# Performance work log

Hardware: AMD Instinct MI355X
Metric: run time of the kernel (lower is better)

The kernel has to match this reference:

```python
import jax, jax.numpy as jnp
import numpy as np

H = 2048      # hidden_size
I = 8192      # dense intermediate_size
MI = 1024     # moe_intermediate_size
E = 8         # num_local_experts
K = 2         # num_experts_per_tok
B, S = 2, 1024
EPS = 1e-6
ROOT = H ** (-0.5)


def _rms(x, w=None, eps=EPS):
    # fp32 RMSNorm matching _Gemma4CPURMSNorm; w=None -> no-scale variant
    ms = jnp.mean(x * x, axis=-1, keepdims=True) + eps
    y = x * jax.lax.rsqrt(ms)
    return y * w if w is not None else y


def _gelu_tanh(x):
    # gelu_pytorch_tanh == tanh-approximate gelu
    return jax.nn.gelu(x, approximate=True)


def setup_inputs() -> dict:
    key = jax.random.key(0)
    ks = jax.random.split(key, 10)
    s = 0.02
    return {
        "hidden_states": jax.random.normal(ks[0], (B, S, H), jnp.float32),
        # RMSNorm scales (init ones, as in nn.Parameter(torch.ones(dim)))
        "rn_pre1": jnp.ones((H,), jnp.float32),
        "rn_pre2": jnp.ones((H,), jnp.float32),
        "rn_post1": jnp.ones((H,), jnp.float32),
        "rn_post2": jnp.ones((H,), jnp.float32),
        "rn_post": jnp.ones((H,), jnp.float32),
        # dense GLU MLP weights, stored (in, out)
        "w_gate": jax.random.normal(ks[1], (H, I), jnp.float32) * s,
        "w_up":   jax.random.normal(ks[2], (H, I), jnp.float32) * s,
        "w_down": jax.random.normal(ks[3], (I, H), jnp.float32) * s,
        # router
        "router_w": jax.random.normal(ks[4], (H, E), jnp.float32) * s,
        "router_scale": jnp.ones((H,), jnp.float32),
        "per_expert_scale": jnp.ones((E,), jnp.float32),
        # per-expert GLU weights, stacked over experts
        "we_gate": jax.random.normal(ks[5], (E, H, MI), jnp.float32) * s,
        "we_up":   jax.random.normal(ks[6], (E, H, MI), jnp.float32) * s,
        "we_down": jax.random.normal(ks[7], (E, MI, H), jnp.float32) * s,
    }


def reference(hidden_states, rn_pre1, rn_pre2, rn_post1, rn_post2, rn_post,
              w_gate, w_up, w_down, router_w, router_scale, per_expert_scale,
              we_gate, we_up, we_down):
    b, s, h = hidden_states.shape
    T = b * s

    # --- dense branch ---
    dense_in = _rms(hidden_states, rn_pre1)                      # (B,S,H)
    dense_out = (_gelu_tanh(dense_in @ w_gate) * (dense_in @ w_up)) @ w_down
    dense_out = _rms(dense_out, rn_post1)                        # (B,S,H)

    # --- router (takes the raw residual, applies its own no-scale RMSNorm) ---
    x = hidden_states.reshape(T, h)
    xr = _rms(x) * router_scale * ROOT                           # (T,H)
    router_logits = xr @ router_w                                # (T,E)
    probs = jax.nn.softmax(router_logits, axis=-1)
    top_w, top_i = jax.lax.top_k(probs, K)                       # (T,K)
    top_w = top_w / jnp.sum(top_w, axis=-1, keepdims=True)
    top_w = top_w * per_expert_scale[top_i]
    aff = jnp.zeros((T, E), x.dtype).at[jnp.arange(T)[:, None], top_i].set(top_w)

    # --- MoE experts (compute all experts, combine with sparse affinities) ---
    moe_in = _rms(hidden_states, rn_pre2).reshape(T, h)          # (T,H)
    g = jnp.einsum('th,ehm->tem', moe_in, we_gate)               # (T,E,MI)
    u = jnp.einsum('th,ehm->tem', moe_in, we_up)
    eo = jnp.einsum('tem,emh->teh', _gelu_tanh(g) * u, we_down)  # (T,E,H)
    moe_out = jnp.einsum('te,teh->th', aff, eo).reshape(b, s, h)
    moe_out = _rms(moe_out, rn_post2)

    return _rms(dense_out + moe_out, rn_post)
```

## Files before the change

kernel.cpp:

```cpp
#include <hip/hip_runtime.h>
#include <stdint.h>

#define TOK 2048
#define HD  2048
#define ID  8192
#define ID2 16384
#define MID 1024
#define NE  8
#define KSPLIT 4

typedef __attribute__((ext_vector_type(8))) short s16x8;
typedef __attribute__((ext_vector_type(4))) short s16x4;
typedef __attribute__((ext_vector_type(4))) float f32x4;

constexpr float EPSF  = 1e-6f;
constexpr float ROOTF = 0.02209708691207961f;

#define MFMA(a, b, c) __builtin_amdgcn_mfma_f32_16x16x32_bf16(a, b, c, 0, 0, 0)
#define BAR() __builtin_amdgcn_s_barrier()
#define SCHED0() __builtin_amdgcn_sched_barrier(0)
#define VMCNT(n) asm volatile("s_waitcnt vmcnt(" #n ")" ::: "memory")

__device__ __forceinline__ void gload16(const void* g, void* l) {
  __builtin_amdgcn_global_load_lds(
      (const __attribute__((address_space(1))) void*)g,
      (__attribute__((address_space(3))) void*)l, 16, 0, 0);
}

__device__ __forceinline__ short f2bf(float f) {
  union { float f; uint32_t u; } v; v.f = f;
  uint32_t r = v.u + 0x7fffu + ((v.u >> 16) & 1u);
  return (short)(r >> 16);
}

__device__ __forceinline__ float bf2f(short s) {
  union { uint32_t u; float f; } v; v.u = ((uint32_t)(uint16_t)s) << 16;
  return v.f;
}

__device__ __forceinline__ float gelu_tanh(float x) {
  float x3 = x * x * x;
  float u = 0.7978845608028654f * (x + 0.044715f * x3);
  return 0.5f * x * (1.0f + tanhf(u));
}

__global__ __launch_bounds__(256) void k_rms_router(
    const float* __restrict__ x, const float* __restrict__ rnp1,
    const float* __restrict__ rnp2, const float* __restrict__ rsc,
    const float* __restrict__ rw, const float* __restrict__ pes,
    short* __restrict__ rms1, short* __restrict__ rms2,
    int* __restrict__ cnt, int* __restrict__ tokl,
    float* __restrict__ wgtl, int* __restrict__ slotl) {
  const int t = blockIdx.x, tid = threadIdx.x;
  const size_t base = (size_t)t * HD;
  f32x4 v[2];
  float ss = 0.f;
#pragma unroll
  for (int i = 0; i < 2; ++i) {
    v[i] = *(const f32x4*)(x + base + tid * 4 + i * 1024);
#pragma unroll
    for (int j = 0; j < 4; ++j) ss += v[i][j] * v[i][j];
  }
  __shared__ float sr[4];
  __shared__ float sl[32];
#pragma unroll
  for (int off = 32; off; off >>= 1) ss += __shfl_down(ss, off, 64);
  if ((tid & 63) == 0) sr[tid >> 6] = ss;
  __syncthreads();
  const float inv = rsqrtf((sr[0] + sr[1] + sr[2] + sr[3]) * (1.0f / HD) + EPSF);
  float p[8] = {0, 0, 0, 0, 0, 0, 0, 0};
#pragma unroll
  for (int i = 0; i < 2; ++i) {
    const int h = tid * 4 + i * 1024;
    f32x4 w1 = *(const f32x4*)(rnp1 + h);
    f32x4 w2 = *(const f32x4*)(rnp2 + h);
    f32x4 sc = *(const f32x4*)(rsc + h);
    s16x4 o1, o2;
#pragma unroll
    for (int j = 0; j < 4; ++j) {
      float xn = v[i][j] * inv;
      o1[j] = f2bf(xn * w1[j]);
      o2[j] = f2bf(xn * w2[j]);
      float xq = xn * sc[j] * ROOTF;
      const float* rr = rw + (size_t)(h + j) * NE;
      f32x4 ra = *(const f32x4*)rr;
      f32x4 rb = *(const f32x4*)(rr + 4);
      p[0] += xq * ra[0]; p[1] += xq * ra[1]; p[2] += xq * ra[2]; p[3] += xq * ra[3];
      p[4] += xq * rb[0]; p[5] += xq * rb[1]; p[6] += xq * rb[2]; p[7] += xq * rb[3];
    }
    *(s16x4*)(rms1 + base + h) = o1;
    *(s16x4*)(rms2 + base + h) = o2;
  }
#pragma unroll
  for (int e = 0; e < 8; ++e)
#pragma unroll
    for (int off = 32; off; off >>= 1) p[e] += __shfl_down(p[e], off, 64);
  if ((tid & 63) == 0) {
#pragma unroll
    for (int e = 0; e < 8; ++e) sl[(tid >> 6) * 8 + e] = p[e];
  }
  __syncthreads();
  if (tid == 0) {
    float l[8];
#pragma unroll
    for (int e = 0; e < 8; ++e) l[e] = sl[e] + sl[8 + e] + sl[16 + e] + sl[24 + e];
    int i1 = 0;
#pragma unroll
    for (int e = 1; e < 8; ++e) if (l[e] > l[i1]) i1 = e;
    int i2 = (i1 == 0) ? 1 : 0;
#pragma unroll
    for (int e = 0; e < 8; ++e) if (e != i1 && l[e] > l[i2]) i2 = e;
    float p2 = expf(l[i2] - l[i1]);
    float s = 1.0f + p2;
    float w1 = (1.0f / s) * pes[i1];
    float w2 = (p2 / s) * pes[i2];
    int q1 = atomicAdd(&cnt[i1], 1);
    tokl[i1 * TOK + q1] = t; wgtl[i1 * TOK + q1] = w1; slotl[i1 * TOK + q1] = 0;
    int q2 = atomicAdd(&cnt[i2], 1);
    tokl[i2 * TOK + q2] = t; wgtl[i2 * TOK + q2] = w2; slotl[i2 * TOK + q2] = 1;
  }
}

__global__ __launch_bounds__(256) void k_transpose(
    const float* __restrict__ in, short* __restrict__ out, int R, int C) {
  __shared__ float tile[64 * 65];
  const int tid = threadIdx.x;
  const int c0 = blockIdx.x * 64, r0 = blockIdx.y * 64;
  const size_t bo = (size_t)blockIdx.z * R * C;
#pragma unroll
  for (int i = 0; i < 4; ++i) {
    int idx = tid + 256 * i;
    int r = idx >> 4, c4 = idx & 15;
    f32x4 f = *(const f32x4*)(in + bo + (size_t)(r0 + r) * C + c0 + c4 * 4);
#pragma unroll
    for (int j = 0; j < 4; ++j) tile[(c4 * 4 + j) * 65 + r] = f[j];
  }
  __syncthreads();
#pragma unroll
  for (int i = 0; i < 2; ++i) {
    int ch = tid + 256 * i;
    int c = ch >> 3, rs = ch & 7;
    s16x8 o;
#pragma unroll
    for (int q = 0; q < 8; ++q) o[q] = f2bf(tile[c * 65 + rs * 8 + q]);
    *(s16x8*)(out + bo + (size_t)(c0 + c) * R + r0 + rs * 8) = o;
  }
}

__global__ __launch_bounds__(512, 2) void k_gemm256(
    const short* __restrict__ Wt,
    const short* __restrict__ X,
    short* __restrict__ C) {
  __shared__ char lds[2][65536];
  const int tid = threadIdx.x;
  const int lane = tid & 63, wave = tid >> 6;
  const int wr = wave >> 2, wc = wave & 3;
  const int ln15 = lane & 15, l16 = lane >> 4;
  const int m0 = blockIdx.x * 256, t0 = blockIdx.y * 256;
  const int swz = (ln15 & 7) << 4;
  const int srow = tid >> 3;
  const int sslot = ((tid & 7) ^ ((tid >> 3) & 7)) << 4;
  const char* Wb = (const char*)Wt;
  const char* Xb = (const char*)X;
  auto STAGE = [&](int kt, int s) {
#pragma unroll
    for (int c = 0; c < 4; ++c) {
      gload16(Wb + (size_t)(m0 + c * 64 + srow) * 4096 + kt * 128 + sslot,
              &lds[s][c * 8192] + wave * 1024);
      gload16(Xb + (size_t)(t0 + c * 64 + srow) * 4096 + kt * 128 + sslot,
              &lds[s][32768 + c * 8192] + wave * 1024);
    }
  };
  f32x4 acc[8][4];
#pragma unroll
  for (int m = 0; m < 8; ++m)
#pragma unroll
    for (int n = 0; n < 4; ++n) acc[m][n] = (f32x4)0.f;
  const int NT = HD / 64;
  STAGE(0, 0);
  STAGE(1, 1);
  VMCNT(8);
  SCHED0();
  BAR();
#pragma unroll 2
  for (int kt = 0; kt < NT; ++kt) {
    const int s = kt & 1;
    const char* sA = &lds[s][0];
    const char* sB = &lds[s][32768];
#pragma unroll
    for (int mh = 0; mh < 2; ++mh)
#pragma unroll
      for (int ks = 0; ks < 2; ++ks) {
        const int ka = (ks * 64 + l16 * 16) ^ swz;
        s16x8 a[4], b[4];
#pragma unroll
        for (int f = 0; f < 4; ++f)
          a[f] = *(const s16x8*)(sA + (wr * 128 + mh * 64 + f * 16 + ln15) * 128 + ka);
#pragma unroll
        for (int n = 0; n < 4; ++n)
          b[n] = *(const s16x8*)(sB + (wc * 64 + n * 16 + ln15) * 128 + ka);
        __builtin_amdgcn_s_setprio(1);
#pragma unroll
        for (int f = 0; f < 4; ++f)
#pragma unroll
          for (int n = 0; n < 4; ++n)
            acc[mh * 4 + f][n] = MFMA(a[f], b[n], acc[mh * 4 + f][n]);
        __builtin_amdgcn_s_setprio(0);
      }
    BAR();
    if (kt + 2 < NT) {
      STAGE(kt + 2, s);
      VMCNT(8);
    } else if (kt + 1 < NT) {
      VMCNT(0);
    }
    SCHED0();
    BAR();
  }
#pragma unroll
  for (int mi = 0; mi < 8; ++mi)
#pragma unroll
    for (int n = 0; n < 4; ++n) {
      const int t = t0 + wc * 64 + n * 16 + ln15;
      const int i = m0 + wr * 128 + mi * 16 + l16 * 4;
      s16x4 o;
#pragma unroll
      for (int r = 0; r < 4; ++r) o[r] = f2bf(acc[mi][n][r]);
      *(s16x4*)(C + (size_t)t * ID2 + i) = o;
    }
}

__global__ __launch_bounds__(512, 2) void k_dd256(
    const short* __restrict__ Wd,
    const short* __restrict__ X,
    float* __restrict__ dparts) {
  __shared__ char lds[2][65536];
  const int tid = threadIdx.x;
  const int lane = tid & 63, wave = tid >> 6;
  const int wr = wave >> 2, wc = wave & 3;
  const int ln15 = lane & 15, l16 = lane >> 4;
  const int m0 = blockIdx.x * 256, t0 = blockIdx.y * 256;
  const size_t kB = (size_t)blockIdx.z * 4096;
  const int swz = (ln15 & 7) << 4;
  const int srow = tid >> 3;
  const int sslot = ((tid & 7) ^ ((tid >> 3) & 7)) << 4;
  const char* Wb = (const char*)Wd;
  const char* Xb = (const char*)X;
  auto STAGE = [&](int kt, int s) {
#pragma unroll
    for (int c = 0; c < 4; ++c) {
      gload16(Wb + (size_t)(m0 + c * 64 + srow) * 16384 + kB + kt * 128 + sslot,
              &lds[s][c * 8192] + wave * 1024);
      gload16(Xb + (size_t)(t0 + c * 64 + srow) * 16384 + kB + kt * 128 + sslot,
              &lds[s][32768 + c * 8192] + wave * 1024);
    }
  };
  f32x4 acc[8][4];
#pragma unroll
  for (int m = 0; m < 8; ++m)
#pragma unroll
    for (int n = 0; n < 4; ++n) acc[m][n] = (f32x4)0.f;
  const int NT = (ID / KSPLIT) / 64;
  STAGE(0, 0);
  STAGE(1, 1);
  VMCNT(8);
  SCHED0();
  BAR();
#pragma unroll 2
  for (int kt = 0; kt < NT; ++kt) {
    const int s = kt & 1;
    const char* sA = &lds[s][0];
    const char* sB = &lds[s][32768];
#pragma unroll
    for (int mh = 0; mh < 2; ++mh)
#pragma unroll
      for (int ks = 0; ks < 2; ++ks) {
        const int ka = (ks * 64 + l16 * 16) ^ swz;
        s16x8 a[4], b[4];
#pragma unroll
        for (int f = 0; f < 4; ++f)
          a[f] = *(const s16x8*)(sA + (wr * 128 + mh * 64 + f * 16 + ln15) * 128 + ka);
#pragma unroll
        for (int n = 0; n < 4; ++n)
          b[n] = *(const s16x8*)(sB + (wc * 64 + n * 16 + ln15) * 128 + ka);
        __builtin_amdgcn_s_setprio(1);
#pragma unroll
        for (int f = 0; f < 4; ++f)
#pragma unroll
          for (int n = 0; n < 4; ++n)
            acc[mh * 4 + f][n] = MFMA(a[f], b[n], acc[mh * 4 + f][n]);
        __builtin_amdgcn_s_setprio(0);
      }
    BAR();
    if (kt + 2 < NT) {
      STAGE(kt + 2, s);
      VMCNT(8);
    } else if (kt + 1 < NT) {
      VMCNT(0);
    }
    SCHED0();
    BAR();
  }
  float* dst = dparts + (size_t)blockIdx.z * TOK * HD;
#pragma unroll
  for (int mi = 0; mi < 8; ++mi)
#pragma unroll
    for (int n = 0; n < 4; ++n) {
      const int t = t0 + wc * 64 + n * 16 + ln15;
      const int h = m0 + wr * 128 + mi * 16 + l16 * 4;
      *(f32x4*)(dst + (size_t)t * HD + h) = acc[mi][n];
    }
}

__global__ __launch_bounds__(256) void k_gelumul(
    const short* __restrict__ cbuf, short* __restrict__ o) {
  const int flat = blockIdx.x * 256 + threadIdx.x;
  const int t = flat >> 10;
  const int i8 = (flat & 1023) * 8;
  const short* g = cbuf + (size_t)t * ID2 + i8;
  s16x8 gv = *(const s16x8*)g;
  s16x8 uv = *(const s16x8*)(g + ID);
  s16x8 ov;
#pragma unroll
  for (int j = 0; j < 8; ++j)
    ov[j] = f2bf(gelu_tanh(bf2f(gv[j])) * bf2f(uv[j]));
  *(s16x8*)(o + (size_t)t * ID + i8) = ov;
}

__global__ __launch_bounds__(256) void k_exp_gateup(
    const short* __restrict__ wegT, const short* __restrict__ weuT,
    const short* __restrict__ rms2,
    const int* __restrict__ cnt, const int* __restrict__ tokl,
    short* __restrict__ acte) {
  const int e = blockIdx.z;
  const int cn = cnt[e];
  const int t0 = blockIdx.y * 128;
  if (t0 >= cn) return;
  const int n0 = blockIdx.x * 64;
  __shared__ short sW[128 * 32];
  __shared__ short sX[128 * 32];
  const int tid = threadIdx.x;
  const int lane = tid & 63, wave = tid >> 6;
  const int ln15 = lane & 15, k8 = (lane >> 4) * 8;
  const int nsub = (wave & 1) * 32, tsub = (wave >> 1) * 64;
  const int srow = tid >> 2, skc = (tid & 3) * 8;
  const int* tl = tokl + e * TOK;
  int r0 = t0 + srow, r1 = t0 + 64 + srow;
  int tk0 = tl[r0 < cn ? r0 : cn - 1];
  int tk1 = tl[r1 < cn ? r1 : cn - 1];
  const short* gW0 = wegT + (size_t)e * MID * HD + (size_t)(n0 + srow) * HD + skc;
  const short* gW1 = weuT + (size_t)e * MID * HD + (size_t)(n0 + srow) * HD + skc;
  const short* gX0 = rms2 + (size_t)tk0 * HD + skc;
  const short* gX1 = rms2 + (size_t)tk1 * HD + skc;
  char* lW = (char*)sW + wave * 1024;
  char* lX = (char*)sX + wave * 1024;
  f32x4 accg[2][4], accu[2][4];
#pragma unroll
  for (int m = 0; m < 2; ++m)
#pragma unroll
    for (int n = 0; n < 4; ++n) { accg[m][n] = (f32x4)0.f; accu[m][n] = (f32x4)0.f; }
  for (int kt = 0; kt < HD / 32; ++kt) {
    const int ko = kt * 32;
    __syncthreads();
    gload16(gW0 + ko, lW);
    gload16(gW1 + ko, lW + 4096);
    gload16(gX0 + ko, lX);
    gload16(gX1 + ko, lX + 4096);
    __syncthreads();
    s16x8 ag[2], au[2], bx[4];
#pragma unroll
    for (int m = 0; m < 2; ++m) {
      ag[m] = *(const s16x8*)(sW + (nsub + m * 16 + ln15) * 32 + k8);
      au[m] = *(const s16x8*)(sW + (64 + nsub + m * 16 + ln15) * 32 + k8);
    }
#pragma unroll
    for (int n = 0; n < 4; ++n)
      bx[n] = *(const s16x8*)(sX + (tsub + n * 16 + ln15) * 32 + k8);
#pragma unroll
    for (int m = 0; m < 2; ++m)
#pragma unroll
      for (int n = 0; n < 4; ++n) {
        accg[m][n] = MFMA(ag[m], bx[n], accg[m][n]);
        accu[m][n] = MFMA(au[m], bx[n], accu[m][n]);
      }
  }
#pragma unroll
  for (int m = 0; m < 2; ++m)
#pragma unroll
    for (int n = 0; n < 4; ++n) {
      const int r = t0 + tsub + n * 16 + ln15;
      if (r < cn) {
        const int ib = n0 + nsub + m * 16 + (lane >> 4) * 4;
        s16x4 o;
#pragma unroll
        for (int q = 0; q < 4; ++q)
          o[q] = f2bf(gelu_tanh(accg[m][n][q]) * accu[m][n][q]);
        *(s16x4*)(acte + (size_t)e * TOK * MID + (size_t)r * MID + ib) = o;
      }
    }
}

__global__ __launch_bounds__(256) void k_exp_down(
    const short* __restrict__ wedT,
    const short* __restrict__ acte,
    const int* __restrict__ cnt, const int* __restrict__ tokl,
    const float* __restrict__ wgtl, const int* __restrict__ slotl,
    float* __restrict__ moep) {
  const int e = blockIdx.z;
  const int cn = cnt[e];
  const int t0 = blockIdx.y * 128;
  if (t0 >= cn) return;
  const int n0 = blockIdx.x * 128;
  __shared__ short sW[128 * 32];
  __shared__ short sX[128 * 32];
  const int tid = threadIdx.x;
  const int lane = tid & 63, wave = tid >> 6;
  const int wr = wave >> 1, wc = wave & 1;
  const int ln15 = lane & 15, k8 = (lane >> 4) * 8;
  const int srow = tid >> 2, skc = (tid & 3) * 8;
  const short* wb = wedT + (size_t)e * HD * MID;
  const short* gW0 = wb + (size_t)(n0 + srow) * MID + skc;
  const short* gW1 = wb + (size_t)(n0 + 64 + srow) * MID + skc;
  const short* ab = acte + (size_t)e * TOK * MID;
  const short* gX0 = ab + (size_t)(t0 + srow) * MID + skc;
  const short* gX1 = ab + (size_t)(t0 + 64 + srow) * MID + skc;
  char* lW = (char*)sW + wave * 1024;
  char* lX = (char*)sX + wave * 1024;
  f32x4 acc[4][4];
#pragma unroll
  for (int m = 0; m < 4; ++m)
#pragma unroll
    for (int n = 0; n < 4; ++n) acc[m][n] = (f32x4)0.f;
  for (int kt = 0; kt < MID / 32; ++kt) {
    const int ko = kt * 32;
    __syncthreads();
    gload16(gW0 + ko, lW);
    gload16(gW1 + ko, lW + 4096);
    gload16(gX0 + ko, lX);
    gload16(gX1 + ko, lX + 4096);
    __syncthreads();
    s16x8 a[4], b[4];
#pragma unroll
    for (int m = 0; m < 4; ++m)
      a[m] = *(const s16x8*)(sW + (wr * 64 + m * 16 + ln15) * 32 + k8);
#pragma unroll
    for (int n = 0; n < 4; ++n)
      b[n] = *(const s16x8*)(sX + (wc * 64 + n * 16 + ln15) * 32 + k8);
#pragma unroll
    for (int m = 0; m < 4; ++m)
#pragma unroll
      for (int n = 0; n < 4; ++n) acc[m][n] = MFMA(a[m], b[n], acc[m][n]);
  }
#pragma unroll
  for (int n = 0; n < 4; ++n) {
    const int r = t0 + wc * 64 + n * 16 + ln15;
    if (r < cn) {
      const int tk = tokl[e * TOK + r];
      const float wf = wgtl[e * TOK + r];
      const int sl = slotl[e * TOK + r];
      float* dst = moep + (size_t)sl * TOK * HD + (size_t)tk * HD;
#pragma unroll
      for (int m = 0; m < 4; ++m) {
        const int h = n0 + wr * 64 + m * 16 + (lane >> 4) * 4;
        f32x4 v = acc[m][n] * wf;
        *(f32x4*)(dst + h) = v;
      }
    }
  }
}

__global__ __launch_bounds__(256) void k_final(
    const float* __restrict__ dparts, const float* __restrict__ moep,
    const float* __restrict__ rno1, const float* __restrict__ rno2,
    const float* __restrict__ rnof, float* __restrict__ out) {
  const int t = blockIdx.x, tid = threadIdx.x;
  const size_t base = (size_t)t * HD;
  f32x4 dv[2], mv[2];
  float ssd = 0.f, ssm = 0.f;
#pragma unroll
  for (int i = 0; i < 2; ++i) {
    const int h = tid * 4 + i * 1024;
    dv[i] = (f32x4)0.f;
#pragma unroll
    for (int z = 0; z < KSPLIT; ++z)
      dv[i] += *(const f32x4*)(dparts + (size_t)z * TOK * HD + base + h);
    f32x4 a = *(const f32x4*)(moep + base + h);
    f32x4 b = *(const f32x4*)(moep + (size_t)TOK * HD + base + h);
    mv[i] = a + b;
#pragma unroll
    for (int j = 0; j < 4; ++j) { ssd += dv[i][j] * dv[i][j]; ssm += mv[i][j] * mv[i][j]; }
  }
  __shared__ float sr[8];
#pragma unroll
  for (int off = 32; off; off >>= 1) {
    ssd += __shfl_down(ssd, off, 64);
    ssm += __shfl_down(ssm, off, 64);
  }
  if ((tid & 63) == 0) { sr[tid >> 6] = ssd; sr[4 + (tid >> 6)] = ssm; }
  __syncthreads();
  const float invd = rsqrtf((sr[0] + sr[1] + sr[2] + sr[3]) * (1.0f / HD) + EPSF);
  const float invm = rsqrtf((sr[4] + sr[5] + sr[6] + sr[7]) * (1.0f / HD) + EPSF);
  f32x4 y[2];
  float ssy = 0.f;
#pragma unroll
  for (int i = 0; i < 2; ++i) {
    const int h = tid * 4 + i * 1024;
    f32x4 w1 = *(const f32x4*)(rno1 + h);
    f32x4 w2 = *(const f32x4*)(rno2 + h);
#pragma unroll
    for (int j = 0; j < 4; ++j) {
      y[i][j] = dv[i][j] * invd * w1[j] + mv[i][j] * invm * w2[j];
      ssy += y[i][j] * y[i][j];
    }
  }
  __syncthreads();
#pragma unroll
  for (int off = 32; off; off >>= 1) ssy += __shfl_down(ssy, off, 64);
  if ((tid & 63) == 0) sr[tid >> 6] = ssy;
  __syncthreads();
  const float invy = rsqrtf((sr[0] + sr[1] + sr[2] + sr[3]) * (1.0f / HD) + EPSF);
#pragma unroll
  for (int i = 0; i < 2; ++i) {
    const int h = tid * 4 + i * 1024;
    f32x4 w = *(const f32x4*)(rnof + h);
    f32x4 o;
#pragma unroll
    for (int j = 0; j < 4; ++j) o[j] = y[i][j] * invy * w[j];
    *(f32x4*)(out + base + h) = o;
  }
}

extern "C" void kernel_launch(void* const* d_in, const int* in_sizes, int n_in,
                              void* d_out, int out_size, void* d_ws, size_t ws_size,
                              hipStream_t stream) {
  (void)in_sizes; (void)n_in; (void)out_size;
  const float* x    = (const float*)d_in[0];
  const float* rnp1 = (const float*)d_in[1];
  const float* rnp2 = (const float*)d_in[2];
  const float* rno1 = (const float*)d_in[3];
  const float* rno2 = (const float*)d_in[4];
  const float* rnof = (const float*)d_in[5];
  const float* wg   = (const float*)d_in[6];
  const float* wu   = (const float*)d_in[7];
  const float* wd   = (const float*)d_in[8];
  const float* rw   = (const float*)d_in[9];
  const float* rsc  = (const float*)d_in[10];
  const float* pes  = (const float*)d_in[11];
  const float* weg  = (const float*)d_in[12];
  const float* weu  = (const float*)d_in[13];
  const float* wed  = (const float*)d_in[14];
  float* out = (float*)d_out;

  char* ws = (char*)d_ws;
  size_t off = 0;
  auto alloc = [&](size_t bytes) -> void* {
    void* p = ws + off;
    off += (bytes + 255) & ~(size_t)255;
    return p;
  };
  const size_t IH  = (size_t)ID * HD;
  const size_t EMH = (size_t)NE * MID * HD;
  short* wgT   = (short*)alloc(IH * 2);
  short* wuT   = (short*)alloc(IH * 2);
  short* wdT   = (short*)alloc(IH * 2);
  short* wegT  = (short*)alloc(EMH * 2);
  short* weuT  = (short*)alloc(EMH * 2);
  short* wedT  = (short*)alloc(EMH * 2);
  short* rms1  = (short*)alloc((size_t)TOK * HD * 2);
  short* rms2  = (short*)alloc((size_t)TOK * HD * 2);
  short* actb  = (short*)alloc((size_t)TOK * ID * 2);
  short* acte  = (short*)alloc((size_t)NE * TOK * MID * 2);
  float* moep  = (float*)alloc((size_t)2 * TOK * HD * 4);
  int*   cnt   = (int*)alloc(NE * 4);
  int*   tokl  = (int*)alloc((size_t)NE * TOK * 4);
  float* wgtl  = (float*)alloc((size_t)NE * TOK * 4);
  int*   slotl = (int*)alloc((size_t)NE * TOK * 4);
  if (off > ws_size) return;
  float* dparts = (float*)wgT;
  short* cbuf = acte;

  hipMemsetAsync(cnt, 0, NE * 4, stream);
  k_rms_router<<<TOK, 256, 0, stream>>>(x, rnp1, rnp2, rsc, rw, pes,
                                        rms1, rms2, cnt, tokl, wgtl, slotl);
  k_transpose<<<dim3(ID / 64, HD / 64, 1), 256, 0, stream>>>(wg, wgT, HD, ID);
  k_transpose<<<dim3(ID / 64, HD / 64, 1), 256, 0, stream>>>(wu, wuT, HD, ID);
  k_transpose<<<dim3(HD / 64, ID / 64, 1), 256, 0, stream>>>(wd, wdT, ID, HD);
  k_transpose<<<dim3(MID / 64, HD / 64, NE), 256, 0, stream>>>(weg, wegT, HD, MID);
  k_transpose<<<dim3(MID / 64, HD / 64, NE), 256, 0, stream>>>(weu, weuT, HD, MID);
  k_transpose<<<dim3(HD / 64, MID / 64, NE), 256, 0, stream>>>(wed, wedT, MID, HD);
  k_gemm256<<<dim3(ID2 / 256, TOK / 256), 512, 0, stream>>>(wgT, rms1, cbuf);
  k_gelumul<<<(TOK * ID) / (256 * 8), 256, 0, stream>>>(cbuf, actb);
  k_dd256<<<dim3(HD / 256, TOK / 256, KSPLIT), 512, 0, stream>>>(wdT, actb, dparts);
  k_exp_gateup<<<dim3(MID / 64, TOK / 128, NE), 256, 0, stream>>>(wegT, weuT, rms2,
                                                                  cnt, tokl, acte);
  k_exp_down<<<dim3(HD / 128, TOK / 128, NE), 256, 0, stream>>>(wedT, acte, cnt, tokl,
                                                                wgtl, slotl, moep);
  k_final<<<TOK, 256, 0, stream>>>(dparts, moep, rno1, rno2, rnof, out);
}
```

Measured before the change: 551.5 us.

## Port expert GEMMs to 256x256 pipelined MFMA kernels and store dense split-K partials as bf16

Replaces the small 128-tile expert gate/up and down kernels with 256x256, 512-thread, double-buffered, swizzled-LDS GEMMs modeled on the dense path. Gate and up now run as two launches, with the second fusing gelu*up into its epilogue by reading back a bf16 gate buffer. The inner loop in all big GEMMs is reordered so B fragments load once per k-step, and the dense split-K partials are written in bf16 instead of fp32 to halve that traffic. The costs are bf16 rounding of partial sums, an extra gate-buffer round trip, and many idle 256-token tiles for experts with few tokens.

```diff
diff --git a/kernel.cpp b/kernel.cpp
--- a/kernel.cpp
+++ b/kernel.cpp
@@ -188,17 +188,18 @@
     const char* sA = &lds[s][0];
     const char* sB = &lds[s][32768];
 #pragma unroll
-    for (int mh = 0; mh < 2; ++mh)
-#pragma unroll
-      for (int ks = 0; ks < 2; ++ks) {
-        const int ka = (ks * 64 + l16 * 16) ^ swz;
-        s16x8 a[4], b[4];
+    for (int ks = 0; ks < 2; ++ks) {
+      const int ka = (ks * 64 + l16 * 16) ^ swz;
+      s16x8 b[4];
+#pragma unroll
+      for (int n = 0; n < 4; ++n)
+        b[n] = *(const s16x8*)(sB + (wc * 64 + n * 16 + ln15) * 128 + ka);
+#pragma unroll
+      for (int mh = 0; mh < 2; ++mh) {
+        s16x8 a[4];
 #pragma unroll
         for (int f = 0; f < 4; ++f)
           a[f] = *(const s16x8*)(sA + (wr * 128 + mh * 64 + f * 16 + ln15) * 128 + ka);
-#pragma unroll
-        for (int n = 0; n < 4; ++n)
-          b[n] = *(const s16x8*)(sB + (wc * 64 + n * 16 + ln15) * 128 + ka);
         __builtin_amdgcn_s_setprio(1);
 #pragma unroll
         for (int f = 0; f < 4; ++f)
@@ -207,6 +208,7 @@
             acc[mh * 4 + f][n] = MFMA(a[f], b[n], acc[mh * 4 + f][n]);
         __builtin_amdgcn_s_setprio(0);
       }
+    }
     BAR();
     if (kt + 2 < NT) {
       STAGE(kt + 2, s);
@@ -233,7 +235,7 @@
 __global__ __launch_bounds__(512, 2) void k_dd256(
     const short* __restrict__ Wd,
     const short* __restrict__ X,
-    float* __restrict__ dparts) {
+    short* __restrict__ dparts) {
   __shared__ char lds[2][65536];
   const int tid = threadIdx.x;
   const int lane = tid & 63, wave = tid >> 6;
@@ -272,17 +274,18 @@
     const char* sA = &lds[s][0];
     const char* sB = &lds[s][32768];
 #pragma unroll
-    for (int mh = 0; mh < 2; ++mh)
-#pragma unroll
-      for (int ks = 0; ks < 2; ++ks) {
-        const int ka = (ks * 64 + l16 * 16) ^ swz;
-        s16x8 a[4], b[4];
+    for (int ks = 0; ks < 2; ++ks) {
+      const int ka = (ks * 64 + l16 * 16) ^ swz;
+      s16x8 b[4];
+#pragma unroll
+      for (int n = 0; n < 4; ++n)
+        b[n] = *(const s16x8*)(sB + (wc * 64 + n * 16 + ln15) * 128 + ka);
+#pragma unroll
+      for (int mh = 0; mh < 2; ++mh) {
+        s16x8 a[4];
 #pragma unroll
         for (int f = 0; f < 4; ++f)
           a[f] = *(const s16x8*)(sA + (wr * 128 + mh * 64 + f * 16 + ln15) * 128 + ka);
-#pragma unroll
-        for (int n = 0; n < 4; ++n)
-          b[n] = *(const s16x8*)(sB + (wc * 64 + n * 16 + ln15) * 128 + ka);
         __builtin_amdgcn_s_setprio(1);
 #pragma unroll
         for (int f = 0; f < 4; ++f)
@@ -291,6 +294,7 @@
             acc[mh * 4 + f][n] = MFMA(a[f], b[n], acc[mh * 4 + f][n]);
         __builtin_amdgcn_s_setprio(0);
       }
+    }
     BAR();
     if (kt + 2 < NT) {
       STAGE(kt + 2, s);
@@ -301,14 +305,17 @@
     SCHED0();
     BAR();
   }
-  float* dst = dparts + (size_t)blockIdx.z * TOK * HD;
+  short* dst = dparts + (size_t)blockIdx.z * TOK * HD;
 #pragma unroll
   for (int mi = 0; mi < 8; ++mi)
 #pragma unroll
     for (int n = 0; n < 4; ++n) {
       const int t = t0 + wc * 64 + n * 16 + ln15;
       const int h = m0 + wr * 128 + mi * 16 + l16 * 4;
-      *(f32x4*)(dst + (size_t)t * HD + h) = acc[mi][n];
+      s16x4 o;
+#pragma unroll
+      for (int r = 0; r < 4; ++r) o[r] = f2bf(acc[mi][n][r]);
+      *(s16x4*)(dst + (size_t)t * HD + h) = o;
     }
 }
 
@@ -327,129 +334,193 @@
   *(s16x8*)(o + (size_t)t * ID + i8) = ov;
 }
 
-__global__ __launch_bounds__(256) void k_exp_gateup(
-    const short* __restrict__ wegT, const short* __restrict__ weuT,
-    const short* __restrict__ rms2,
+__global__ __launch_bounds__(512, 2) void k_eg256(
+    const short* __restrict__ W,
+    const short* __restrict__ X,
     const int* __restrict__ cnt, const int* __restrict__ tokl,
-    short* __restrict__ acte) {
+    short* __restrict__ gout,
+    short* __restrict__ aout,
+    int fuse) {
+  __shared__ char lds[2][65536];
   const int e = blockIdx.z;
   const int cn = cnt[e];
-  const int t0 = blockIdx.y * 128;
+  const int t0 = blockIdx.y * 256;
   if (t0 >= cn) return;
-  const int n0 = blockIdx.x * 64;
-  __shared__ short sW[128 * 32];
-  __shared__ short sX[128 * 32];
   const int tid = threadIdx.x;
   const int lane = tid & 63, wave = tid >> 6;
-  const int ln15 = lane & 15, k8 = (lane >> 4) * 8;
-  const int nsub = (wave & 1) * 32, tsub = (wave >> 1) * 64;
-  const int srow = tid >> 2, skc = (tid & 3) * 8;
+  const int wr = wave >> 2, wc = wave & 3;
+  const int ln15 = lane & 15, l16 = lane >> 4;
+  const int m0 = blockIdx.x * 256;
+  const int swz = (ln15 & 7) << 4;
+  const int srow = tid >> 3;
+  const int sslot = ((tid & 7) ^ ((tid >> 3) & 7)) << 4;
+  const char* Wb = (const char*)(W + (size_t)e * MID * HD + (size_t)m0 * HD);
+  const char* Xb = (const char*)X;
   const int* tl = tokl + e * TOK;
-  int r0 = t0 + srow, r1 = t0 + 64 + srow;
-  int tk0 = tl[r0 < cn ? r0 : cn - 1];
-  int tk1 = tl[r1 < cn ? r1 : cn - 1];
-  const short* gW0 = wegT + (size_t)e * MID * HD + (size_t)(n0 + srow) * HD + skc;
-  const short* gW1 = weuT + (size_t)e * MID * HD + (size_t)(n0 + srow) * HD + skc;
-  const short* gX0 = rms2 + (size_t)tk0 * HD + skc;
-  const short* gX1 = rms2 + (size_t)tk1 * HD + skc;
-  char* lW = (char*)sW + wave * 1024;
-  char* lX = (char*)sX + wave * 1024;
-  f32x4 accg[2][4], accu[2][4];
-#pragma unroll
-  for (int m = 0; m < 2; ++m)
-#pragma unroll
-    for (int n = 0; n < 4; ++n) { accg[m][n] = (f32x4)0.f; accu[m][n] = (f32x4)0.f; }
-  for (int kt = 0; kt < HD / 32; ++kt) {
-    const int ko = kt * 32;
-    __syncthreads();
-    gload16(gW0 + ko, lW);
-    gload16(gW1 + ko, lW + 4096);
-    gload16(gX0 + ko, lX);
-    gload16(gX1 + ko, lX + 4096);
-    __syncthreads();
-    s16x8 ag[2], au[2], bx[4];
-#pragma unroll
-    for (int m = 0; m < 2; ++m) {
-      ag[m] = *(const s16x8*)(sW + (nsub + m * 16 + ln15) * 32 + k8);
-      au[m] = *(const s16x8*)(sW + (64 + nsub + m * 16 + ln15) * 32 + k8);
-    }
-#pragma unroll
-    for (int n = 0; n < 4; ++n)
-      bx[n] = *(const s16x8*)(sX + (tsub + n * 16 + ln15) * 32 + k8);
-#pragma unroll
-    for (int m = 0; m < 2; ++m)
-#pragma unroll
-      for (int n = 0; n < 4; ++n) {
-        accg[m][n] = MFMA(ag[m], bx[n], accg[m][n]);
-        accu[m][n] = MFMA(au[m], bx[n], accu[m][n]);
+  int tk[4];
+#pragma unroll
+  for (int c = 0; c < 4; ++c) {
+    int r = t0 + c * 64 + srow;
+    tk[c] = tl[r < cn ? r : cn - 1];
+  }
+  auto STAGE = [&](int kt, int s) {
+#pragma unroll
+    for (int c = 0; c < 4; ++c) {
+      gload16(Wb + (size_t)(c * 64 + srow) * 4096 + kt * 128 + sslot,
+              &lds[s][c * 8192] + wave * 1024);
+      gload16(Xb + (size_t)tk[c] * 4096 + kt * 128 + sslot,
+              &lds[s][32768 + c * 8192] + wave * 1024);
+    }
+  };
+  f32x4 acc[8][4];
+#pragma unroll
+  for (int m = 0; m < 8; ++m)
+#pragma unroll
+    for (int n = 0; n < 4; ++n) acc[m][n] = (f32x4)0.f;
+  const int NT = HD / 64;
+  STAGE(0, 0);
+  STAGE(1, 1);
+  VMCNT(8);
+  SCHED0();
+  BAR();
+#pragma unroll 2
+  for (int kt = 0; kt < NT; ++kt) {
+    const int s = kt & 1;
+    const char* sA = &lds[s][0];
+    const char* sB = &lds[s][32768];
+#pragma unroll
+    for (int ks = 0; ks < 2; ++ks) {
+      const int ka = (ks * 64 + l16 * 16) ^ swz;
+      s16x8 b[4];
+#pragma unroll
+      for (int n = 0; n < 4; ++n)
+        b[n] = *(const s16x8*)(sB + (wc * 64 + n * 16 + ln15) * 128 + ka);
+#pragma unroll
+      for (int mh = 0; mh < 2; ++mh) {
+        s16x8 a[4];
+#pragma unroll
+        for (int f = 0; f < 4; ++f)
+          a[f] = *(const s16x8*)(sA + (wr * 128 + mh * 64 + f * 16 + ln15) * 128 + ka);
+        __builtin_amdgcn_s_setprio(1);
+#pragma unroll
+        for (int f = 0; f < 4; ++f)
+#pragma unroll
+          for (int n = 0; n < 4; ++n)
+            acc[mh * 4 + f][n] = MFMA(a[f], b[n], acc[mh * 4 + f][n]);
+        __builtin_amdgcn_s_setprio(0);
       }
-  }
-#pragma unroll
-  for (int m = 0; m < 2; ++m)
+    }
+    BAR();
+    if (kt + 2 < NT) {
+      STAGE(kt + 2, s);
+      VMCNT(8);
+    } else if (kt + 1 < NT) {
+      VMCNT(0);
+    }
+    SCHED0();
+    BAR();
+  }
+#pragma unroll
+  for (int mi = 0; mi < 8; ++mi)
 #pragma unroll
     for (int n = 0; n < 4; ++n) {
-      const int r = t0 + tsub + n * 16 + ln15;
+      const int r = t0 + wc * 64 + n * 16 + ln15;
       if (r < cn) {
-        const int ib = n0 + nsub + m * 16 + (lane >> 4) * 4;
+        const int m = m0 + wr * 128 + mi * 16 + l16 * 4;
+        const size_t off = (size_t)e * TOK * MID + (size_t)r * MID + m;
         s16x4 o;
-#pragma unroll
-        for (int q = 0; q < 4; ++q)
-          o[q] = f2bf(gelu_tanh(accg[m][n][q]) * accu[m][n][q]);
-        *(s16x4*)(acte + (size_t)e * TOK * MID + (size_t)r * MID + ib) = o;
+        if (fuse) {
+          s16x4 g4 = *(const s16x4*)(gout + off);
+#pragma unroll
+          for (int j = 0; j < 4; ++j)
+            o[j] = f2bf(gelu_tanh(bf2f(g4[j])) * acc[mi][n][j]);
+          *(s16x4*)(aout + off) = o;
+        } else {
+#pragma unroll
+          for (int j = 0; j < 4; ++j) o[j] = f2bf(acc[mi][n][j]);
+          *(s16x4*)(gout + off) = o;
+        }
       }
     }
 }
 
-__global__ __launch_bounds__(256) void k_exp_down(
-    const short* __restrict__ wedT,
-    const short* __restrict__ acte,
+__global__ __launch_bounds__(512, 2) void k_ed256(
+    const short* __restrict__ W,
+    const short* __restrict__ A2,
     const int* __restrict__ cnt, const int* __restrict__ tokl,
     const float* __restrict__ wgtl, const int* __restrict__ slotl,
     float* __restrict__ moep) {
+  __shared__ char lds[2][65536];
   const int e = blockIdx.z;
   const int cn = cnt[e];
-  const int t0 = blockIdx.y * 128;
+  const int t0 = blockIdx.y * 256;
   if (t0 >= cn) return;
-  const int n0 = blockIdx.x * 128;
-  __shared__ short sW[128 * 32];
-  __shared__ short sX[128 * 32];
   const int tid = threadIdx.x;
   const int lane = tid & 63, wave = tid >> 6;
-  const int wr = wave >> 1, wc = wave & 1;
-  const int ln15 = lane & 15, k8 = (lane >> 4) * 8;
-  const int srow = tid >> 2, skc = (tid & 3) * 8;
-  const short* wb = wedT + (size_t)e * HD * MID;
-  const short* gW0 = wb + (size_t)(n0 + srow) * MID + skc;
-  const short* gW1 = wb + (size_t)(n0 + 64 + srow) * MID + skc;
-  const short* ab = acte + (size_t)e * TOK * MID;
-  const short* gX0 = ab + (size_t)(t0 + srow) * MID + skc;
-  const short* gX1 = ab + (size_t)(t0 + 64 + srow) * MID + skc;
-  char* lW = (char*)sW + wave * 1024;
-  char* lX = (char*)sX + wave * 1024;
-  f32x4 acc[4][4];
-#pragma unroll
-  for (int m = 0; m < 4; ++m)
+  const int wr = wave >> 2, wc = wave & 3;
+  const int ln15 = lane & 15, l16 = lane >> 4;
+  const int m0 = blockIdx.x * 256;
+  const int swz = (ln15 & 7) << 4;
+  const int srow = tid >> 3;
+  const int sslot = ((tid & 7) ^ ((tid >> 3) & 7)) << 4;
+  const char* Wb = (const char*)(W + (size_t)e * HD * MID + (size_t)m0 * MID);
+  const char* Xb = (const char*)(A2 + (size_t)e * TOK * MID + (size_t)t0 * MID);
+  auto STAGE = [&](int kt, int s) {
+#pragma unroll
+    for (int c = 0; c < 4; ++c) {
+      gload16(Wb + (size_t)(c * 64 + srow) * 2048 + kt * 128 + sslot,
+              &lds[s][c * 8192] + wave * 1024);
+      gload16(Xb + (size_t)(c * 64 + srow) * 2048 + kt * 128 + sslot,
+              &lds[s][32768 + c * 8192] + wave * 1024);
+    }
+  };
+  f32x4 acc[8][4];
+#pragma unroll
+  for (int m = 0; m < 8; ++m)
 #pragma unroll
     for (int n = 0; n < 4; ++n) acc[m][n] = (f32x4)0.f;
-  for (int kt = 0; kt < MID / 32; ++kt) {
-    const int ko = kt * 32;
-    __syncthreads();
-    gload16(gW0 + ko, lW);
-    gload16(gW1 + ko, lW + 4096);
-    gload16(gX0 + ko, lX);
-    gload16(gX1 + ko, lX + 4096);
-    __syncthreads();
-    s16x8 a[4], b[4];
-#pragma unroll
-    for (int m = 0; m < 4; ++m)
-      a[m] = *(const s16x8*)(sW + (wr * 64 + m * 16 + ln15) * 32 + k8);
-#pragma unroll
-    for (int n = 0; n < 4; ++n)
-      b[n] = *(const s16x8*)(sX + (wc * 64 + n * 16 + ln15) * 32 + k8);
-#pragma unroll
-    for (int m = 0; m < 4; ++m)
-#pragma unroll
-      for (int n = 0; n < 4; ++n) acc[m][n] = MFMA(a[m], b[n], acc[m][n]);
+  const int NT = MID / 64;
+  STAGE(0, 0);
+  STAGE(1, 1);
+  VMCNT(8);
+  SCHED0();
+  BAR();
+#pragma unroll 2
+  for (int kt = 0; kt < NT; ++kt) {
+    const int s = kt & 1;
+    const char* sA = &lds[s][0];
+    const char* sB = &lds[s][32768];
+#pragma unroll
+    for (int ks = 0; ks < 2; ++ks) {
+      const int ka = (ks * 64 + l16 * 16) ^ swz;
+      s16x8 b[4];
+#pragma unroll
+      for (int n = 0; n < 4; ++n)
+        b[n] = *(const s16x8*)(sB + (wc * 64 + n * 16 + ln15) * 128 + ka);
+#pragma unroll
+      for (int mh = 0; mh < 2; ++mh) {
+        s16x8 a[4];
+#pragma unroll
+        for (int f = 0; f < 4; ++f)
+          a[f] = *(const s16x8*)(sA + (wr * 128 + mh * 64 + f * 16 + ln15) * 128 + ka);
+        __builtin_amdgcn_s_setprio(1);
+#pragma unroll
+        for (int f = 0; f < 4; ++f)
+#pragma unroll
+          for (int n = 0; n < 4; ++n)
+            acc[mh * 4 + f][n] = MFMA(a[f], b[n], acc[mh * 4 + f][n]);
+        __builtin_amdgcn_s_setprio(0);
+      }
+    }
+    BAR();
+    if (kt + 2 < NT) {
+      STAGE(kt + 2, s);
+      VMCNT(8);
+    } else if (kt + 1 < NT) {
+      VMCNT(0);
+    }
+    SCHED0();
+    BAR();
   }
 #pragma unroll
   for (int n = 0; n < 4; ++n) {
@@ -460,9 +531,9 @@
       const int sl = slotl[e * TOK + r];
       float* dst = moep + (size_t)sl * TOK * HD + (size_t)tk * HD;
 #pragma unroll
-      for (int m = 0; m < 4; ++m) {
-        const int h = n0 + wr * 64 + m * 16 + (lane >> 4) * 4;
-        f32x4 v = acc[m][n] * wf;
+      for (int mi = 0; mi < 8; ++mi) {
+        const int h = m0 + wr * 128 + mi * 16 + l16 * 4;
+        f32x4 v = acc[mi][n] * wf;
         *(f32x4*)(dst + h) = v;
       }
     }
@@ -470,7 +541,8 @@
 }
 
 __global__ __launch_bounds__(256) void k_final(
-    const float* __restrict__ dparts, const float* __restrict__ moep,
+    const short* __restrict__ dparts,
+    const float* __restrict__ moep,
     const float* __restrict__ rno1, const float* __restrict__ rno2,
     const float* __restrict__ rnof, float* __restrict__ out) {
   const int t = blockIdx.x, tid = threadIdx.x;
@@ -482,8 +554,11 @@
     const int h = tid * 4 + i * 1024;
     dv[i] = (f32x4)0.f;
 #pragma unroll
-    for (int z = 0; z < KSPLIT; ++z)
-      dv[i] += *(const f32x4*)(dparts + (size_t)z * TOK * HD + base + h);
+    for (int z = 0; z < KSPLIT; ++z) {
+      s16x4 d4 = *(const s16x4*)(dparts + (size_t)z * TOK * HD + base + h);
+#pragma unroll
+      for (int j = 0; j < 4; ++j) dv[i][j] += bf2f(d4[j]);
+    }
     f32x4 a = *(const f32x4*)(moep + base + h);
     f32x4 b = *(const f32x4*)(moep + (size_t)TOK * HD + base + h);
     mv[i] = a + b;
@@ -576,8 +651,10 @@
   float* wgtl  = (float*)alloc((size_t)NE * TOK * 4);
   int*   slotl = (int*)alloc((size_t)NE * TOK * 4);
   if (off > ws_size) return;
-  float* dparts = (float*)wgT;
+  short* dparts = (short*)wgT;
   short* cbuf = acte;
+  short* graw = actb;
+  short* acte2 = acte;
 
   hipMemsetAsync(cnt, 0, NE * 4, stream);
   k_rms_router<<<TOK, 256, 0, stream>>>(x, rnp1, rnp2, rsc, rw, pes,
@@ -591,9 +668,11 @@
   k_gemm256<<<dim3(ID2 / 256, TOK / 256), 512, 0, stream>>>(wgT, rms1, cbuf);
   k_gelumul<<<(TOK * ID) / (256 * 8), 256, 0, stream>>>(cbuf, actb);
   k_dd256<<<dim3(HD / 256, TOK / 256, KSPLIT), 512, 0, stream>>>(wdT, actb, dparts);
-  k_exp_gateup<<<dim3(MID / 64, TOK / 128, NE), 256, 0, stream>>>(wegT, weuT, rms2,
-                                                                  cnt, tokl, acte);
-  k_exp_down<<<dim3(HD / 128, TOK / 128, NE), 256, 0, stream>>>(wedT, acte, cnt, tokl,
-                                                                wgtl, slotl, moep);
+  k_eg256<<<dim3(MID / 256, TOK / 256, NE), 512, 0, stream>>>(wegT, rms2, cnt, tokl,
+                                                              graw, acte2, 0);
+  k_eg256<<<dim3(MID / 256, TOK / 256, NE), 512, 0, stream>>>(weuT, rms2, cnt, tokl,
+                                                              graw, acte2, 1);
+  k_ed256<<<dim3(HD / 256, TOK / 256, NE), 512, 0, stream>>>(wedT, acte2, cnt, tokl,
+                                                             wgtl, slotl, moep);
   k_final<<<TOK, 256, 0, stream>>>(dparts, moep, rno1, rno2, rnof, out);
 }
```

New measurement: 645.1 us. +17.0%, slower.

## Swizzle gate/up GEMM block order, hoist B fragments, store down-proj partials as bf16

Applied to the files above, without the earlier changes.

Three changes. The gate/up GEMM remaps its block index so consecutive blocks share row tiles, aiming for better L2 reuse. Both 256-tile GEMMs reorder the inner loops so B fragments are loaded from LDS once per k-step and reused across both M halves, cutting LDS reads. The split-K partials of the dense down projection are written as bf16 instead of fp32, halving that write and read traffic, at the cost of extra rounding before the final RMSNorm.

```diff
diff --git a/kernel.cpp b/kernel.cpp
--- a/kernel.cpp
+++ b/kernel.cpp
@@ -156,7 +156,9 @@
   const int lane = tid & 63, wave = tid >> 6;
   const int wr = wave >> 2, wc = wave & 3;
   const int ln15 = lane & 15, l16 = lane >> 4;
-  const int m0 = blockIdx.x * 256, t0 = blockIdx.y * 256;
+  const int lin = blockIdx.y * 64 + blockIdx.x;
+  const int lin2 = (lin & 7) * 64 + (lin >> 3);
+  const int m0 = (lin2 & 63) * 256, t0 = (lin2 >> 6) * 256;
   const int swz = (ln15 & 7) << 4;
   const int srow = tid >> 3;
   const int sslot = ((tid & 7) ^ ((tid >> 3) & 7)) << 4;
@@ -188,17 +190,18 @@
     const char* sA = &lds[s][0];
     const char* sB = &lds[s][32768];
 #pragma unroll
-    for (int mh = 0; mh < 2; ++mh)
-#pragma unroll
-      for (int ks = 0; ks < 2; ++ks) {
-        const int ka = (ks * 64 + l16 * 16) ^ swz;
-        s16x8 a[4], b[4];
+    for (int ks = 0; ks < 2; ++ks) {
+      const int ka = (ks * 64 + l16 * 16) ^ swz;
+      s16x8 b[4];
+#pragma unroll
+      for (int n = 0; n < 4; ++n)
+        b[n] = *(const s16x8*)(sB + (wc * 64 + n * 16 + ln15) * 128 + ka);
+#pragma unroll
+      for (int mh = 0; mh < 2; ++mh) {
+        s16x8 a[4];
 #pragma unroll
         for (int f = 0; f < 4; ++f)
           a[f] = *(const s16x8*)(sA + (wr * 128 + mh * 64 + f * 16 + ln15) * 128 + ka);
-#pragma unroll
-        for (int n = 0; n < 4; ++n)
-          b[n] = *(const s16x8*)(sB + (wc * 64 + n * 16 + ln15) * 128 + ka);
         __builtin_amdgcn_s_setprio(1);
 #pragma unroll
         for (int f = 0; f < 4; ++f)
@@ -207,6 +210,7 @@
             acc[mh * 4 + f][n] = MFMA(a[f], b[n], acc[mh * 4 + f][n]);
         __builtin_amdgcn_s_setprio(0);
       }
+    }
     BAR();
     if (kt + 2 < NT) {
       STAGE(kt + 2, s);
@@ -233,7 +237,7 @@
 __global__ __launch_bounds__(512, 2) void k_dd256(
     const short* __restrict__ Wd,
     const short* __restrict__ X,
-    float* __restrict__ dparts) {
+    short* __restrict__ dparts) {
   __shared__ char lds[2][65536];
   const int tid = threadIdx.x;
   const int lane = tid & 63, wave = tid >> 6;
@@ -272,17 +276,18 @@
     const char* sA = &lds[s][0];
     const char* sB = &lds[s][32768];
 #pragma unroll
-    for (int mh = 0; mh < 2; ++mh)
-#pragma unroll
-      for (int ks = 0; ks < 2; ++ks) {
-        const int ka = (ks * 64 + l16 * 16) ^ swz;
-        s16x8 a[4], b[4];
+    for (int ks = 0; ks < 2; ++ks) {
+      const int ka = (ks * 64 + l16 * 16) ^ swz;
+      s16x8 b[4];
+#pragma unroll
+      for (int n = 0; n < 4; ++n)
+        b[n] = *(const s16x8*)(sB + (wc * 64 + n * 16 + ln15) * 128 + ka);
+#pragma unroll
+      for (int mh = 0; mh < 2; ++mh) {
+        s16x8 a[4];
 #pragma unroll
         for (int f = 0; f < 4; ++f)
           a[f] = *(const s16x8*)(sA + (wr * 128 + mh * 64 + f * 16 + ln15) * 128 + ka);
-#pragma unroll
-        for (int n = 0; n < 4; ++n)
-          b[n] = *(const s16x8*)(sB + (wc * 64 + n * 16 + ln15) * 128 + ka);
         __builtin_amdgcn_s_setprio(1);
 #pragma unroll
         for (int f = 0; f < 4; ++f)
@@ -291,6 +296,7 @@
             acc[mh * 4 + f][n] = MFMA(a[f], b[n], acc[mh * 4 + f][n]);
         __builtin_amdgcn_s_setprio(0);
       }
+    }
     BAR();
     if (kt + 2 < NT) {
       STAGE(kt + 2, s);
@@ -301,14 +307,17 @@
     SCHED0();
     BAR();
   }
-  float* dst = dparts + (size_t)blockIdx.z * TOK * HD;
+  short* dst = dparts + (size_t)blockIdx.z * TOK * HD;
 #pragma unroll
   for (int mi = 0; mi < 8; ++mi)
 #pragma unroll
     for (int n = 0; n < 4; ++n) {
       const int t = t0 + wc * 64 + n * 16 + ln15;
       const int h = m0 + wr * 128 + mi * 16 + l16 * 4;
-      *(f32x4*)(dst + (size_t)t * HD + h) = acc[mi][n];
+      s16x4 o;
+#pragma unroll
+      for (int r = 0; r < 4; ++r) o[r] = f2bf(acc[mi][n][r]);
+      *(s16x4*)(dst + (size_t)t * HD + h) = o;
     }
 }
 
@@ -470,7 +479,8 @@
 }
 
 __global__ __launch_bounds__(256) void k_final(
-    const float* __restrict__ dparts, const float* __restrict__ moep,
+    const short* __restrict__ dparts,
+    const float* __restrict__ moep,
     const float* __restrict__ rno1, const float* __restrict__ rno2,
     const float* __restrict__ rnof, float* __restrict__ out) {
   const int t = blockIdx.x, tid = threadIdx.x;
@@ -482,8 +492,11 @@
     const int h = tid * 4 + i * 1024;
     dv[i] = (f32x4)0.f;
 #pragma unroll
-    for (int z = 0; z < KSPLIT; ++z)
-      dv[i] += *(const f32x4*)(dparts + (size_t)z * TOK * HD + base + h);
+    for (int z = 0; z < KSPLIT; ++z) {
+      s16x4 d4 = *(const s16x4*)(dparts + (size_t)z * TOK * HD + base + h);
+#pragma unroll
+      for (int j = 0; j < 4; ++j) dv[i][j] += bf2f(d4[j]);
+    }
     f32x4 a = *(const f32x4*)(moep + base + h);
     f32x4 b = *(const f32x4*)(moep + (size_t)TOK * HD + base + h);
     mv[i] = a + b;
@@ -576,7 +589,7 @@
   float* wgtl  = (float*)alloc((size_t)NE * TOK * 4);
   int*   slotl = (int*)alloc((size_t)NE * TOK * 4);
   if (off > ws_size) return;
-  float* dparts = (float*)wgT;
+  short* dparts = (short*)wgT;
   short* cbuf = acte;
 
   hipMemsetAsync(cnt, 0, NE * 4, stream);
```

After: 554.6 us. No clear change (+0.6%).
